# Optimization experiments

Hardware: AMD Instinct MI355X
Metric: run time of the kernel (lower is better)

Reference implementation:

```python
import jax, jax.numpy as jnp
import numpy as np

B, S, H, NH = 4, 2048, 1024, 16
D = H // NH  # d_per_head = 64


def setup_inputs() -> dict:
    key = jax.random.key(0)
    ks = jax.random.split(key, 6)
    return {
        "x": jax.random.normal(ks[0], (B, S, H), dtype=jnp.float32),
        "W_query": jax.random.uniform(ks[1], (NH, D, H), dtype=jnp.float32),
        "W_key": jax.random.uniform(ks[2], (NH, D, H), dtype=jnp.float32),
        "W_value": jax.random.uniform(ks[3], (NH, D, H), dtype=jnp.float32),
        "W_out": jax.random.normal(ks[4], (H, H), dtype=jnp.float32) * 0.02,
        "b_out": jnp.zeros((H,), dtype=jnp.float32),
    }


def reference(x, W_query, W_key, W_value, W_out, b_out):
    b, s, h = x.shape
    n_head, d, _ = W_query.shape
    # ALiBi: slope_i = -(i+1); distance[q, k] = k - q (non-causal, full softmax)
    dist = (jnp.arange(s)[None, :] - jnp.arange(s)[:, None]).astype(x.dtype)  # [s, s]
    slopes = -(jnp.arange(1, n_head + 1, dtype=x.dtype))  # [n_head]
    # per-head projections: x @ W[i].T  -> [b, n, s, d]
    q = jnp.einsum("bsh,ndh->bnsd", x, W_query)
    k = jnp.einsum("bsh,ndh->bnsd", x, W_key)
    v = jnp.einsum("bsh,ndh->bnsd", x, W_value)
    scores = jnp.einsum("bnqd,bnkd->bnqk", q, k) / jnp.sqrt(jnp.asarray(d, x.dtype))
    scores = scores + slopes[None, :, None, None] * dist[None, None, :, :]
    attn = jax.nn.softmax(scores, axis=-1)
    heads = jnp.einsum("bnqk,bnkd->bnqd", attn, v)  # [b, n, s, d]
    # concat heads along feature dim (head 0 first, matching torch cat order)
    multi = heads.transpose(0, 2, 1, 3).reshape(b, s, n_head * d)
    return multi @ W_out.T + b_out
```

## Files before the change

kernel.cpp:

```cpp
#include <hip/hip_runtime.h>
#include <hip/hip_bf16.h>
#include <stdint.h>

typedef unsigned short u16;
typedef short bf16x8 __attribute__((ext_vector_type(8)));
typedef float f32x4 __attribute__((ext_vector_type(4)));
typedef uint32_t u32x4 __attribute__((ext_vector_type(4)));

#define DEV __device__ __forceinline__

DEV u16 f2bf(float f) {
  union { float f; uint32_t u; } v; v.f = f;
  uint32_t u = v.u;
  return (u16)((u + 0x7FFFu + ((u >> 16) & 1u)) >> 16);
}
DEV float bf2f(u16 h) {
  union { uint32_t u; float f; } v; v.u = ((uint32_t)h) << 16;
  return v.f;
}
DEV uint32_t cvtpk_bf16(float lo, float hi) {
  uint32_t r;
  asm volatile("v_cvt_pk_bf16_f32 %0, %1, %2" : "=v"(r) : "v"(lo), "v"(hi));
  return r;
}

#if __has_builtin(__builtin_amdgcn_exp2f)
#define EXP2F(x) __builtin_amdgcn_exp2f(x)
#else
#define EXP2F(x) exp2f(x)
#endif

#define GLL(gp, lp) __builtin_amdgcn_global_load_lds(\
    (const __attribute__((address_space(1))) unsigned int*)(gp), \
    (__attribute__((address_space(3))) unsigned int*)(lp), 16, 0, 0)

__global__ void prep_x(const float* __restrict__ x, u16* __restrict__ xh, u16* __restrict__ xl) {
  int i = blockIdx.x * 256 + threadIdx.x;
  float4 v = ((const float4*)x)[i];
  ushort4 h, lo;
  h.x = f2bf(v.x); h.y = f2bf(v.y); h.z = f2bf(v.z); h.w = f2bf(v.w);
  lo.x = f2bf(v.x - bf2f(h.x)); lo.y = f2bf(v.y - bf2f(h.y));
  lo.z = f2bf(v.z - bf2f(h.z)); lo.w = f2bf(v.w - bf2f(h.w));
  ((ushort4*)xh)[i] = h;
  ((ushort4*)xl)[i] = lo;
}

__global__ void prep_w(const float* __restrict__ wq, const float* __restrict__ wk,
                       const float* __restrict__ wv, const float* __restrict__ wo,
                       u16* __restrict__ wqkh, u16* __restrict__ wqkl,
                       u16* __restrict__ wvb, u16* __restrict__ wob) {
  int i = blockIdx.x * 256 + threadIdx.x;
  int seg = i >> 18;
  int j = i & ((1 << 18) - 1);
  const float* src = (seg == 0) ? wq : (seg == 1) ? wk : (seg == 2) ? wv : wo;
  float4 v = ((const float4*)src)[j];
  ushort4 h;
  h.x = f2bf(v.x); h.y = f2bf(v.y); h.z = f2bf(v.z); h.w = f2bf(v.w);
  if (seg < 2) {
    ushort4 lo;
    lo.x = f2bf(v.x - bf2f(h.x)); lo.y = f2bf(v.y - bf2f(h.y));
    lo.z = f2bf(v.z - bf2f(h.z)); lo.w = f2bf(v.w - bf2f(h.w));
    ((ushort4*)wqkh)[i] = h;
    ((ushort4*)wqkl)[i] = lo;
  } else if (seg == 2) {
    ((ushort4*)wvb)[j] = h;
  } else {
    ((ushort4*)wob)[j] = h;
  }
}

__global__ __launch_bounds__(256, 2) void qkv_gemm(
    const u16* __restrict__ xh, const u16* __restrict__ xl,
    const u16* __restrict__ wh, const u16* __restrict__ wl,
    const u16* __restrict__ wv,
    u16* __restrict__ qkh, u16* __restrict__ qkl, u16* __restrict__ vout) {
  __shared__ u16 Ah[128 * 32], Al[128 * 32], Bh[128 * 32], Bl[128 * 32];
  const int t = threadIdx.x, w = t >> 6, l = t & 63, g = l >> 4, lr = l & 15;
  const int m0 = blockIdx.y * 128, n0 = blockIdx.x * 128;
  const bool split = (n0 < 2048);
  const u16* bsrc_h = split ? (wh + (size_t)n0 * 1024) : (wv + (size_t)(n0 - 2048) * 1024);
  const u16* bsrc_l = split ? (wl + (size_t)n0 * 1024) : wl;
  const int wr = w >> 1, wc = w & 1;
  const int sk = (lr ^ (lr >> 2)) & 3;

  f32x4 zero = {0.f, 0.f, 0.f, 0.f};
  f32x4 acc[4][4];
#pragma unroll
  for (int mi = 0; mi < 4; ++mi)
#pragma unroll
    for (int ni = 0; ni < 4; ++ni) acc[mi][ni] = zero;

  for (int k0 = 0; k0 < 1024; k0 += 32) {
    __syncthreads();
#pragma unroll
    for (int i = 0; i < 2; ++i) {
      const int c = i * 256 + t;
      const int row = c >> 2;
      const int kc8 = ((c & 3) ^ (((c >> 2) ^ (c >> 4)) & 3)) * 8;
      const size_t goff = (size_t)row * 1024 + k0 + kc8;
      const int lo = i * 4096 + w * 1024;
      GLL(xh + (size_t)m0 * 1024 + goff, (char*)Ah + lo);
      GLL(bsrc_h + goff, (char*)Bh + lo);
      if (split) {
        GLL(xl + (size_t)m0 * 1024 + goff, (char*)Al + lo);
        GLL(bsrc_l + goff, (char*)Bl + lo);
      }
    }
    __syncthreads();

    bf16x8 ah[4], al[4];
#pragma unroll
    for (int mi = 0; mi < 4; ++mi) {
      const int idx = (wr * 64 + mi * 16 + lr) * 32 + ((g ^ sk) << 3);
      ah[mi] = *(const bf16x8*)&Ah[idx];
      if (split) al[mi] = *(const bf16x8*)&Al[idx];
    }
#pragma unroll
    for (int ni = 0; ni < 4; ++ni) {
      const int idx = (wc * 64 + ni * 16 + lr) * 32 + ((g ^ sk) << 3);
      bf16x8 bh = *(const bf16x8*)&Bh[idx];
      bf16x8 bl;
      if (split) bl = *(const bf16x8*)&Bl[idx];
#pragma unroll
      for (int mi = 0; mi < 4; ++mi) {
        acc[mi][ni] = __builtin_amdgcn_mfma_f32_16x16x32_bf16(ah[mi], bh, acc[mi][ni], 0, 0, 0);
        if (split) {
          acc[mi][ni] = __builtin_amdgcn_mfma_f32_16x16x32_bf16(al[mi], bh, acc[mi][ni], 0, 0, 0);
          acc[mi][ni] = __builtin_amdgcn_mfma_f32_16x16x32_bf16(ah[mi], bl, acc[mi][ni], 0, 0, 0);
        }
      }
    }
  }

#pragma unroll
  for (int mi = 0; mi < 4; ++mi)
#pragma unroll
    for (int ni = 0; ni < 4; ++ni)
#pragma unroll
      for (int r = 0; r < 4; ++r) {
        const int row = m0 + wr * 64 + mi * 16 + g * 4 + r;
        const int col = wc * 64 + ni * 16 + lr;
        const float cval = acc[mi][ni][r];
        if (split) {
          const u16 h = f2bf(cval);
          qkh[(size_t)row * 2048 + n0 + col] = h;
          qkl[(size_t)row * 2048 + n0 + col] = f2bf(cval - bf2f(h));
        } else {
          vout[(size_t)row * 1024 + (n0 - 2048) + col] = f2bf(cval);
        }
      }
}

__global__ __launch_bounds__(256) void vtrans(const u16* __restrict__ vin, u16* __restrict__ vout) {
  __shared__ u16 Ts[64 * 66];
  const int t = threadIdx.x;
  const int r0 = blockIdx.y * 64, c0 = blockIdx.x * 64;
  const int rl = t >> 3, cc = (t & 7) * 8;
#pragma unroll
  for (int i = 0; i < 2; ++i) {
    const int r = rl + i * 32;
    bf16x8 v = *(const bf16x8*)&vin[(size_t)(r0 + r) * 1024 + c0 + cc];
#pragma unroll
    for (int e = 0; e < 8; ++e) Ts[(cc + e) * 66 + r] = (u16)v[e];
  }
  __syncthreads();
  const int c = t >> 2, seg = (t & 3) * 16;
  u16 tmp[16];
#pragma unroll
  for (int e = 0; e < 16; ++e) tmp[e] = Ts[c * 66 + seg + e];
  *(bf16x8*)&vout[(size_t)(c0 + c) * 8192 + r0 + seg] = *(const bf16x8*)&tmp[0];
  *(bf16x8*)&vout[(size_t)(c0 + c) * 8192 + r0 + seg + 8] = *(const bf16x8*)&tmp[8];
}

__global__ __launch_bounds__(512, 2) void attn(
    const u16* __restrict__ qkh, const u16* __restrict__ qkl,
    const u16* __restrict__ vt, u16* __restrict__ multi) {
  __shared__ u16 Ksh[3][4096], Ksl[3][4096], Vts[3][4096];
  const int t = threadIdx.x, w = t >> 6, l = t & 63, g = l >> 4, lr = l & 15;
  const int L = blockIdx.x;
  const int flat = (L & 7) * 64 + (L >> 3);
  const int b = flat >> 7, h = (flat >> 3) & 15, qt = flat & 7;
  const int q0 = qt * 256;
  const size_t rowbase = (size_t)b * 2048;
  const u16* Qh = qkh + rowbase * 2048 + h * 64;
  const u16* Ql = qkl + rowbase * 2048 + h * 64;
  const u16* Kh = qkh + rowbase * 2048 + 1024 + h * 64;
  const u16* Kl = qkl + rowbase * 2048 + 1024 + h * 64;
  const u16* Vb = vt + (size_t)(h * 64) * 8192 + b * 2048;

  const int srow = l >> 3;
  const int sj = (l & 7) ^ srow;
  const int krow = w * 8 + srow;
  const int klog = ((krow >> 5) << 5) | (((krow >> 2) & 3) << 3)
                 | (((krow >> 4) & 1) << 2) | (krow & 3);
  const int ldsoff = w * 1024;

  bf16x8 qfh[2][2], qfl[2][2];
#pragma unroll
  for (int nt = 0; nt < 2; ++nt)
#pragma unroll
    for (int kc = 0; kc < 2; ++kc) {
      const size_t off = (size_t)(q0 + w * 32 + nt * 16 + lr) * 2048 + kc * 32 + g * 8;
      qfh[nt][kc] = *(const bf16x8*)&Qh[off];
      qfl[nt][kc] = *(const bf16x8*)&Ql[off];
    }

  f32x4 zero = {0.f, 0.f, 0.f, 0.f};
  f32x4 o[2][4];
#pragma unroll
  for (int nt = 0; nt < 2; ++nt)
#pragma unroll
    for (int dn = 0; dn < 4; ++dn) o[nt][dn] = zero;
  float mst[2] = {-3.0e38f, -3.0e38f};
  float lst[2] = {0.f, 0.f};

  const float c1 = 0.125f * 1.44269504088896f;
  const float slope2 = -(float)(h + 1) * 1.44269504088896f;
  const float s2r1 = slope2, s2r2 = slope2 * 2.0f, s2r3 = slope2 * 3.0f;
  float base[4];
#pragma unroll
  for (int mt = 0; mt < 4; ++mt)
    base[mt] = slope2 * (float)(((mt >> 1) << 5) + ((mt & 1) << 2) + g * 8);
  const float bstep = slope2 * 64.0f;

  auto STAGE = [&](int tile, int buf) {
    GLL(Kh + (size_t)(tile * 64 + klog) * 2048 + sj * 8, (char*)&Ksh[buf][0] + ldsoff);
    GLL(Kl + (size_t)(tile * 64 + klog) * 2048 + sj * 8, (char*)&Ksl[buf][0] + ldsoff);
    GLL(Vb + (size_t)krow * 8192 + tile * 64 + sj * 8, (char*)&Vts[buf][0] + ldsoff);
  };

  auto QK = [&](int buf, f32x4 (&c)[4][2]) {
    const u16* Kcur = &Ksh[buf][0];
    const u16* Lcur = &Ksl[buf][0];
#pragma unroll
    for (int mt = 0; mt < 4; ++mt)
#pragma unroll
      for (int nt = 0; nt < 2; ++nt) c[mt][nt] = zero;
    __builtin_amdgcn_s_setprio(1);
#pragma unroll
    for (int mt = 0; mt < 4; ++mt) {
      bf16x8 ah[2], al[2];
#pragma unroll
      for (int kc = 0; kc < 2; ++kc) {
        const int rk = mt * 16 + lr;
        const int byte = rk * 128 + (((kc * 4 + g) ^ (rk & 7)) << 4);
        ah[kc] = *(const bf16x8*)((const char*)Kcur + byte);
        al[kc] = *(const bf16x8*)((const char*)Lcur + byte);
      }
#pragma unroll
      for (int nt = 0; nt < 2; ++nt) {
        f32x4 a = c[mt][nt];
        a = __builtin_amdgcn_mfma_f32_16x16x32_bf16(ah[0], qfh[nt][0], a, 0, 0, 0);
        a = __builtin_amdgcn_mfma_f32_16x16x32_bf16(ah[1], qfh[nt][1], a, 0, 0, 0);
        a = __builtin_amdgcn_mfma_f32_16x16x32_bf16(al[0], qfh[nt][0], a, 0, 0, 0);
        a = __builtin_amdgcn_mfma_f32_16x16x32_bf16(al[1], qfh[nt][1], a, 0, 0, 0);
        a = __builtin_amdgcn_mfma_f32_16x16x32_bf16(ah[0], qfl[nt][0], a, 0, 0, 0);
        a = __builtin_amdgcn_mfma_f32_16x16x32_bf16(ah[1], qfl[nt][1], a, 0, 0, 0);
        c[mt][nt] = a;
      }
    }
    __builtin_amdgcn_s_setprio(0);
  };

  auto SMPV = [&](f32x4 (&c)[4][2], int buf) {
    const u16* Vcur = &Vts[buf][0];
#pragma unroll
    for (int mt = 0; mt < 4; ++mt)
#pragma unroll
      for (int nt = 0; nt < 2; ++nt) {
        f32x4 a = c[mt][nt];
        a[0] = fmaf(a[0], c1, base[mt]);
        a[1] = fmaf(a[1], c1, base[mt] + s2r1);
        a[2] = fmaf(a[2], c1, base[mt] + s2r2);
        a[3] = fmaf(a[3], c1, base[mt] + s2r3);
        c[mt][nt] = a;
      }
    float rmax[2];
#pragma unroll
    for (int nt = 0; nt < 2; ++nt) {
      float m01 = fmaxf(fmaxf(c[0][nt][0], c[0][nt][1]), fmaxf(c[0][nt][2], c[0][nt][3]));
      float m23 = fmaxf(fmaxf(c[1][nt][0], c[1][nt][1]), fmaxf(c[1][nt][2], c[1][nt][3]));
      float m45 = fmaxf(fmaxf(c[2][nt][0], c[2][nt][1]), fmaxf(c[2][nt][2], c[2][nt][3]));
      float m67 = fmaxf(fmaxf(c[3][nt][0], c[3][nt][1]), fmaxf(c[3][nt][2], c[3][nt][3]));
      float m = fmaxf(fmaxf(m01, m23), fmaxf(m45, m67));
      m = fmaxf(m, __shfl_xor(m, 16));
      m = fmaxf(m, __shfl_xor(m, 32));
      rmax[nt] = m;
    }
    const bool needr = (rmax[0] > mst[0]) | (rmax[1] > mst[1]);
    if (__any(needr)) {
#pragma unroll
      for (int nt = 0; nt < 2; ++nt) {
        const float mn = fmaxf(mst[nt], rmax[nt]);
        const float alpha = EXP2F(mst[nt] - mn);
        mst[nt] = mn;
        lst[nt] *= alpha;
#pragma unroll
        for (int dn = 0; dn < 4; ++dn) {
          o[nt][dn][0] *= alpha; o[nt][dn][1] *= alpha;
          o[nt][dn][2] *= alpha; o[nt][dn][3] *= alpha;
        }
      }
    }
    bf16x8 pb[2][2];
#pragma unroll
    for (int nt = 0; nt < 2; ++nt) {
      float rsum = 0.f;
      uint32_t pk01[4], pk23[4];
#pragma unroll
      for (int mt = 0; mt < 4; ++mt) {
        const float p0 = EXP2F(c[mt][nt][0] - mst[nt]);
        const float p1 = EXP2F(c[mt][nt][1] - mst[nt]);
        const float p2 = EXP2F(c[mt][nt][2] - mst[nt]);
        const float p3 = EXP2F(c[mt][nt][3] - mst[nt]);
        rsum += (p0 + p1) + (p2 + p3);
        pk01[mt] = cvtpk_bf16(p0, p1);
        pk23[mt] = cvtpk_bf16(p2, p3);
      }
      rsum += __shfl_xor(rsum, 16);
      rsum += __shfl_xor(rsum, 32);
      lst[nt] += rsum;
      union { u32x4 u; bf16x8 bf; } cv0, cv1;
      cv0.u = (u32x4){pk01[0], pk23[0], pk01[1], pk23[1]};
      cv1.u = (u32x4){pk01[2], pk23[2], pk01[3], pk23[3]};
      pb[nt][0] = cv0.bf;
      pb[nt][1] = cv1.bf;
    }
    __builtin_amdgcn_s_setprio(1);
#pragma unroll
    for (int dn = 0; dn < 4; ++dn) {
      bf16x8 vb[2];
#pragma unroll
      for (int kc = 0; kc < 2; ++kc) {
        const int row = dn * 16 + lr;
        const int jk = kc * 4 + g;
        const int byte = row * 128 + ((jk ^ (row & 7)) << 4);
        vb[kc] = *(const bf16x8*)((const char*)Vcur + byte);
      }
#pragma unroll
      for (int nt = 0; nt < 2; ++nt) {
        o[nt][dn] = __builtin_amdgcn_mfma_f32_16x16x32_bf16(vb[0], pb[nt][0], o[nt][dn], 0, 0, 0);
        o[nt][dn] = __builtin_amdgcn_mfma_f32_16x16x32_bf16(vb[1], pb[nt][1], o[nt][dn], 0, 0, 0);
      }
    }
    __builtin_amdgcn_s_setprio(0);
#pragma unroll
    for (int mt = 0; mt < 4; ++mt) base[mt] += bstep;
  };

  STAGE(0, 0);
  __syncthreads();

  f32x4 cR[4][2];

  for (int kt = 0; kt < 32; ++kt) {
    if (kt + 1 < 32) STAGE(kt + 1, (kt + 1) % 3);
    if (w < 4) {
      QK(kt % 3, cR);
      SMPV(cR, kt % 3);
    } else {
      if (kt > 0) SMPV(cR, (kt + 2) % 3);
      QK(kt % 3, cR);
    }
    __syncthreads();
  }
  if (w >= 4) SMPV(cR, 31 % 3);

#pragma unroll
  for (int nt = 0; nt < 2; ++nt) {
    const float rinv = 1.0f / lst[nt];
    const int qrow = q0 + w * 32 + nt * 16 + lr;
#pragma unroll
    for (int dn = 0; dn < 4; ++dn) {
      uint2 pkv;
      pkv.x = cvtpk_bf16(o[nt][dn][0] * rinv, o[nt][dn][1] * rinv);
      pkv.y = cvtpk_bf16(o[nt][dn][2] * rinv, o[nt][dn][3] * rinv);
      *(uint2*)&multi[(rowbase + qrow) * 1024 + h * 64 + dn * 16 + g * 4] = pkv;
    }
  }
}

__global__ __launch_bounds__(256, 2) void out_gemm(
    const u16* __restrict__ A, const u16* __restrict__ Bw,
    const float* __restrict__ bias, float* __restrict__ out) {
  __shared__ u16 As[128 * 32], Bs[128 * 32];
  const int t = threadIdx.x, w = t >> 6, l = t & 63, g = l >> 4, lr = l & 15;
  const int m0 = blockIdx.y * 128, n0 = blockIdx.x * 128;
  const int wr = w >> 1, wc = w & 1;
  const int sk = (lr ^ (lr >> 2)) & 3;

  f32x4 zero = {0.f, 0.f, 0.f, 0.f};
  f32x4 acc[4][4];
#pragma unroll
  for (int mi = 0; mi < 4; ++mi)
#pragma unroll
    for (int ni = 0; ni < 4; ++ni) acc[mi][ni] = zero;

  for (int k0 = 0; k0 < 1024; k0 += 32) {
    __syncthreads();
#pragma unroll
    for (int i = 0; i < 2; ++i) {
      const int c = i * 256 + t;
      const int row = c >> 2;
      const int kc8 = ((c & 3) ^ (((c >> 2) ^ (c >> 4)) & 3)) * 8;
      const size_t goff = (size_t)row * 1024 + k0 + kc8;
      const int lo = i * 4096 + w * 1024;
      GLL(A + (size_t)m0 * 1024 + goff, (char*)As + lo);
      GLL(Bw + (size_t)n0 * 1024 + goff, (char*)Bs + lo);
    }
    __syncthreads();

    bf16x8 ah[4];
#pragma unroll
    for (int mi = 0; mi < 4; ++mi)
      ah[mi] = *(const bf16x8*)&As[(wr * 64 + mi * 16 + lr) * 32 + ((g ^ sk) << 3)];
#pragma unroll
    for (int ni = 0; ni < 4; ++ni) {
      bf16x8 bh = *(const bf16x8*)&Bs[(wc * 64 + ni * 16 + lr) * 32 + ((g ^ sk) << 3)];
#pragma unroll
      for (int mi = 0; mi < 4; ++mi)
        acc[mi][ni] = __builtin_amdgcn_mfma_f32_16x16x32_bf16(ah[mi], bh, acc[mi][ni], 0, 0, 0);
    }
  }

#pragma unroll
  for (int mi = 0; mi < 4; ++mi)
#pragma unroll
    for (int ni = 0; ni < 4; ++ni)
#pragma unroll
      for (int r = 0; r < 4; ++r) {
        const int row = m0 + wr * 64 + mi * 16 + g * 4 + r;
        const int col = n0 + wc * 64 + ni * 16 + lr;
        out[(size_t)row * 1024 + col] = acc[mi][ni][r] + bias[col];
      }
}

extern "C" void kernel_launch(void* const* d_in, const int* in_sizes, int n_in,
                              void* d_out, int out_size, void* d_ws, size_t ws_size,
                              hipStream_t stream) {
  (void)in_sizes; (void)n_in; (void)out_size; (void)ws_size;
  const float* x  = (const float*)d_in[0];
  const float* wq = (const float*)d_in[1];
  const float* wk = (const float*)d_in[2];
  const float* wv = (const float*)d_in[3];
  const float* wo = (const float*)d_in[4];
  const float* bo = (const float*)d_in[5];
  float* out = (float*)d_out;
  char* ws = (char*)d_ws;

  const size_t MB = 1024 * 1024;
  u16* xh   = (u16*)(ws + 0);
  u16* xl   = (u16*)(ws + 16 * MB);
  u16* qkh  = (u16*)(ws + 32 * MB);
  u16* qkl  = (u16*)(ws + 64 * MB);
  u16* vbf  = (u16*)(ws + 96 * MB);
  u16* wqkh = (u16*)(ws + 112 * MB);
  u16* wqkl = (u16*)(ws + 116 * MB);
  u16* wvb  = (u16*)(ws + 120 * MB);
  u16* wob  = (u16*)(ws + 122 * MB);
  u16* multi = xh;
  u16* vt    = xl;

  prep_x<<<8192, 256, 0, stream>>>(x, xh, xl);
  prep_w<<<4096, 256, 0, stream>>>(wq, wk, wv, wo, wqkh, wqkl, wvb, wob);
  qkv_gemm<<<dim3(24, 64), 256, 0, stream>>>(xh, xl, wqkh, wqkl, wvb, qkh, qkl, vbf);
  vtrans<<<dim3(16, 128), 256, 0, stream>>>(vbf, vt);
  attn<<<512, 512, 0, stream>>>(qkh, qkl, vt, multi);
  out_gemm<<<dim3(8, 64), 256, 0, stream>>>(multi, wob, bo, out);
}
```

Before: 326.5 us.

## Fuse V transpose into QKV GEMM epilogue and merge prep kernels

The V-projection blocks of the QKV GEMM now transpose their bf16 tile through swizzled LDS and write V already transposed, so the separate vtrans kernel and its round trip through global memory go away. The x and weight prep kernels are merged into one launch. This saves two launches and about 16MB of V write/read traffic, at the cost of extra LDS barriers in the GEMM epilogue.

```diff
diff --git a/kernel.cpp b/kernel.cpp
--- a/kernel.cpp
+++ b/kernel.cpp
@@ -34,38 +34,41 @@
     (const __attribute__((address_space(1))) unsigned int*)(gp), \
     (__attribute__((address_space(3))) unsigned int*)(lp), 16, 0, 0)
 
-__global__ void prep_x(const float* __restrict__ x, u16* __restrict__ xh, u16* __restrict__ xl) {
-  int i = blockIdx.x * 256 + threadIdx.x;
-  float4 v = ((const float4*)x)[i];
-  ushort4 h, lo;
-  h.x = f2bf(v.x); h.y = f2bf(v.y); h.z = f2bf(v.z); h.w = f2bf(v.w);
-  lo.x = f2bf(v.x - bf2f(h.x)); lo.y = f2bf(v.y - bf2f(h.y));
-  lo.z = f2bf(v.z - bf2f(h.z)); lo.w = f2bf(v.w - bf2f(h.w));
-  ((ushort4*)xh)[i] = h;
-  ((ushort4*)xl)[i] = lo;
-}
-
-__global__ void prep_w(const float* __restrict__ wq, const float* __restrict__ wk,
-                       const float* __restrict__ wv, const float* __restrict__ wo,
-                       u16* __restrict__ wqkh, u16* __restrict__ wqkl,
-                       u16* __restrict__ wvb, u16* __restrict__ wob) {
-  int i = blockIdx.x * 256 + threadIdx.x;
-  int seg = i >> 18;
-  int j = i & ((1 << 18) - 1);
-  const float* src = (seg == 0) ? wq : (seg == 1) ? wk : (seg == 2) ? wv : wo;
-  float4 v = ((const float4*)src)[j];
-  ushort4 h;
-  h.x = f2bf(v.x); h.y = f2bf(v.y); h.z = f2bf(v.z); h.w = f2bf(v.w);
-  if (seg < 2) {
-    ushort4 lo;
+__global__ void prep(const float* __restrict__ x,
+                     const float* __restrict__ wq, const float* __restrict__ wk,
+                     const float* __restrict__ wv, const float* __restrict__ wo,
+                     u16* __restrict__ xh, u16* __restrict__ xl,
+                     u16* __restrict__ wqkh, u16* __restrict__ wqkl,
+                     u16* __restrict__ wvb, u16* __restrict__ wob) {
+  const int blk = blockIdx.x;
+  if (blk < 8192) {
+    int i = blk * 256 + threadIdx.x;
+    float4 v = ((const float4*)x)[i];
+    ushort4 h, lo;
+    h.x = f2bf(v.x); h.y = f2bf(v.y); h.z = f2bf(v.z); h.w = f2bf(v.w);
     lo.x = f2bf(v.x - bf2f(h.x)); lo.y = f2bf(v.y - bf2f(h.y));
     lo.z = f2bf(v.z - bf2f(h.z)); lo.w = f2bf(v.w - bf2f(h.w));
-    ((ushort4*)wqkh)[i] = h;
-    ((ushort4*)wqkl)[i] = lo;
-  } else if (seg == 2) {
-    ((ushort4*)wvb)[j] = h;
+    ((ushort4*)xh)[i] = h;
+    ((ushort4*)xl)[i] = lo;
   } else {
-    ((ushort4*)wob)[j] = h;
+    int i = (blk - 8192) * 256 + threadIdx.x;
+    int seg = i >> 18;
+    int j = i & ((1 << 18) - 1);
+    const float* src = (seg == 0) ? wq : (seg == 1) ? wk : (seg == 2) ? wv : wo;
+    float4 v = ((const float4*)src)[j];
+    ushort4 h;
+    h.x = f2bf(v.x); h.y = f2bf(v.y); h.z = f2bf(v.z); h.w = f2bf(v.w);
+    if (seg < 2) {
+      ushort4 lo;
+      lo.x = f2bf(v.x - bf2f(h.x)); lo.y = f2bf(v.y - bf2f(h.y));
+      lo.z = f2bf(v.z - bf2f(h.z)); lo.w = f2bf(v.w - bf2f(h.w));
+      ((ushort4*)wqkh)[i] = h;
+      ((ushort4*)wqkl)[i] = lo;
+    } else if (seg == 2) {
+      ((ushort4*)wvb)[j] = h;
+    } else {
+      ((ushort4*)wob)[j] = h;
+    }
   }
 }
 
@@ -73,8 +76,8 @@
     const u16* __restrict__ xh, const u16* __restrict__ xl,
     const u16* __restrict__ wh, const u16* __restrict__ wl,
     const u16* __restrict__ wv,
-    u16* __restrict__ qkh, u16* __restrict__ qkl, u16* __restrict__ vout) {
-  __shared__ u16 Ah[128 * 32], Al[128 * 32], Bh[128 * 32], Bl[128 * 32];
+    u16* __restrict__ qkh, u16* __restrict__ qkl, u16* __restrict__ vt) {
+  __shared__ u16 LDS4[4][4096];
   const int t = threadIdx.x, w = t >> 6, l = t & 63, g = l >> 4, lr = l & 15;
   const int m0 = blockIdx.y * 128, n0 = blockIdx.x * 128;
   const bool split = (n0 < 2048);
@@ -99,11 +102,11 @@
       const int kc8 = ((c & 3) ^ (((c >> 2) ^ (c >> 4)) & 3)) * 8;
       const size_t goff = (size_t)row * 1024 + k0 + kc8;
       const int lo = i * 4096 + w * 1024;
-      GLL(xh + (size_t)m0 * 1024 + goff, (char*)Ah + lo);
-      GLL(bsrc_h + goff, (char*)Bh + lo);
+      GLL(xh + (size_t)m0 * 1024 + goff, (char*)&LDS4[0][0] + lo);
+      GLL(bsrc_h + goff, (char*)&LDS4[1][0] + lo);
       if (split) {
-        GLL(xl + (size_t)m0 * 1024 + goff, (char*)Al + lo);
-        GLL(bsrc_l + goff, (char*)Bl + lo);
+        GLL(xl + (size_t)m0 * 1024 + goff, (char*)&LDS4[2][0] + lo);
+        GLL(bsrc_l + goff, (char*)&LDS4[3][0] + lo);
       }
     }
     __syncthreads();
@@ -112,15 +115,15 @@
 #pragma unroll
     for (int mi = 0; mi < 4; ++mi) {
       const int idx = (wr * 64 + mi * 16 + lr) * 32 + ((g ^ sk) << 3);
-      ah[mi] = *(const bf16x8*)&Ah[idx];
-      if (split) al[mi] = *(const bf16x8*)&Al[idx];
+      ah[mi] = *(const bf16x8*)&LDS4[0][idx];
+      if (split) al[mi] = *(const bf16x8*)&LDS4[2][idx];
     }
 #pragma unroll
     for (int ni = 0; ni < 4; ++ni) {
       const int idx = (wc * 64 + ni * 16 + lr) * 32 + ((g ^ sk) << 3);
-      bf16x8 bh = *(const bf16x8*)&Bh[idx];
+      bf16x8 bh = *(const bf16x8*)&LDS4[1][idx];
       bf16x8 bl;
-      if (split) bl = *(const bf16x8*)&Bl[idx];
+      if (split) bl = *(const bf16x8*)&LDS4[3][idx];
 #pragma unroll
       for (int mi = 0; mi < 4; ++mi) {
         acc[mi][ni] = __builtin_amdgcn_mfma_f32_16x16x32_bf16(ah[mi], bh, acc[mi][ni], 0, 0, 0);
@@ -132,44 +135,58 @@
     }
   }
 
-#pragma unroll
-  for (int mi = 0; mi < 4; ++mi)
-#pragma unroll
-    for (int ni = 0; ni < 4; ++ni)
-#pragma unroll
-      for (int r = 0; r < 4; ++r) {
-        const int row = m0 + wr * 64 + mi * 16 + g * 4 + r;
-        const int col = wc * 64 + ni * 16 + lr;
-        const float cval = acc[mi][ni][r];
-        if (split) {
+  if (split) {
+#pragma unroll
+    for (int mi = 0; mi < 4; ++mi)
+#pragma unroll
+      for (int ni = 0; ni < 4; ++ni)
+#pragma unroll
+        for (int r = 0; r < 4; ++r) {
+          const int row = m0 + wr * 64 + mi * 16 + g * 4 + r;
+          const int col = wc * 64 + ni * 16 + lr;
+          const float cval = acc[mi][ni][r];
           const u16 h = f2bf(cval);
           qkh[(size_t)row * 2048 + n0 + col] = h;
           qkl[(size_t)row * 2048 + n0 + col] = f2bf(cval - bf2f(h));
-        } else {
-          vout[(size_t)row * 1024 + (n0 - 2048) + col] = f2bf(cval);
         }
-      }
-}
-
-__global__ __launch_bounds__(256) void vtrans(const u16* __restrict__ vin, u16* __restrict__ vout) {
-  __shared__ u16 Ts[64 * 66];
-  const int t = threadIdx.x;
-  const int r0 = blockIdx.y * 64, c0 = blockIdx.x * 64;
-  const int rl = t >> 3, cc = (t & 7) * 8;
-#pragma unroll
-  for (int i = 0; i < 2; ++i) {
-    const int r = rl + i * 32;
-    bf16x8 v = *(const bf16x8*)&vin[(size_t)(r0 + r) * 1024 + c0 + cc];
-#pragma unroll
-    for (int e = 0; e < 8; ++e) Ts[(cc + e) * 66 + r] = (u16)v[e];
-  }
-  __syncthreads();
-  const int c = t >> 2, seg = (t & 3) * 16;
-  u16 tmp[16];
-#pragma unroll
-  for (int e = 0; e < 16; ++e) tmp[e] = Ts[c * 66 + seg + e];
-  *(bf16x8*)&vout[(size_t)(c0 + c) * 8192 + r0 + seg] = *(const bf16x8*)&tmp[0];
-  *(bf16x8*)&vout[(size_t)(c0 + c) * 8192 + r0 + seg + 8] = *(const bf16x8*)&tmp[8];
+  } else {
+    const int n0v = n0 - 2048;
+    u16* T = &LDS4[2][0];
+    for (int hh = 0; hh < 2; ++hh) {
+      if (wc == hh) {
+#pragma unroll
+        for (int mi = 0; mi < 4; ++mi)
+#pragma unroll
+          for (int ni = 0; ni < 4; ++ni) {
+            const int c = ni * 16 + lr;
+            const int row0 = wr * 64 + mi * 16 + g * 4;
+            const int sw = (c & 31) << 2;
+            uint2 pk;
+            pk.x = cvtpk_bf16(acc[mi][ni][0], acc[mi][ni][1]);
+            pk.y = cvtpk_bf16(acc[mi][ni][2], acc[mi][ni][3]);
+            *(uint2*)&T[c * 128 + (row0 ^ sw)] = pk;
+          }
+      }
+      __syncthreads();
+      {
+        const int cb = t >> 4;
+        const int sl = t & 15;
+#pragma unroll
+        for (int e = 0; e < 4; ++e) {
+          const int c = cb + e * 16;
+          const int sw = (c & 31) << 2;
+          const int s = sl * 8;
+          const int p0 = s ^ sw;
+          const int p1 = p0 ^ 4;
+          uint2 lo = *(const uint2*)&T[c * 128 + p0];
+          uint2 hi = *(const uint2*)&T[c * 128 + p1];
+          uint4 ov; ov.x = lo.x; ov.y = lo.y; ov.z = hi.x; ov.w = hi.y;
+          *(uint4*)&vt[(size_t)(n0v + hh * 64 + c) * 8192 + m0 + s] = ov;
+        }
+      }
+      __syncthreads();
+    }
+  }
 }
 
 __global__ __launch_bounds__(512, 2) void attn(
@@ -453,18 +470,15 @@
   u16* xl   = (u16*)(ws + 16 * MB);
   u16* qkh  = (u16*)(ws + 32 * MB);
   u16* qkl  = (u16*)(ws + 64 * MB);
-  u16* vbf  = (u16*)(ws + 96 * MB);
+  u16* vt   = (u16*)(ws + 96 * MB);
   u16* wqkh = (u16*)(ws + 112 * MB);
   u16* wqkl = (u16*)(ws + 116 * MB);
   u16* wvb  = (u16*)(ws + 120 * MB);
   u16* wob  = (u16*)(ws + 122 * MB);
   u16* multi = xh;
-  u16* vt    = xl;
-
-  prep_x<<<8192, 256, 0, stream>>>(x, xh, xl);
-  prep_w<<<4096, 256, 0, stream>>>(wq, wk, wv, wo, wqkh, wqkl, wvb, wob);
-  qkv_gemm<<<dim3(24, 64), 256, 0, stream>>>(xh, xl, wqkh, wqkl, wvb, qkh, qkl, vbf);
-  vtrans<<<dim3(16, 128), 256, 0, stream>>>(vbf, vt);
+
+  prep<<<12288, 256, 0, stream>>>(x, wq, wk, wv, wo, xh, xl, wqkh, wqkl, wvb, wob);
+  qkv_gemm<<<dim3(24, 64), 256, 0, stream>>>(xh, xl, wqkh, wqkl, wvb, qkh, qkl, vt);
   attn<<<512, 512, 0, stream>>>(qkh, qkl, vt, multi);
   out_gemm<<<dim3(8, 64), 256, 0, stream>>>(multi, wob, bo, out);
 }
```

Measured after the change: 314.2 us. -3.8%, faster.
